# Kernel tuning notes

Hardware: AMD Instinct MI355X
Metric: run time of the kernel (lower is better)

## Reference

```python
import jax, jax.numpy as jnp
import numpy as np

THRESHOLD = 0.9
EPS = 1e-12  # F.normalize eps


def setup_inputs() -> dict:
    key = jax.random.key(0)
    clusters = jax.random.normal(key, (64, 256, 768), dtype=jnp.float32)
    return {"clusters": clusters}


def _collapse(clusters, threshold):
    B, Q, D = clusters.shape
    # F.normalize(clusters, dim=-1): divide by L2 norm clamped to eps
    norm = jnp.maximum(jnp.linalg.norm(clusters, axis=-1, keepdims=True), EPS)
    nc = clusters / norm
    sim = jnp.einsum('bqd,bkd->bqk', nc, nc)              # [B, Q, Q]
    # torch loop condition: collapse_mask[:, i, j].any() -> any over batch
    pair_flag = jnp.any(sim > threshold, axis=0)          # [Q, Q] bool, fixed before merging

    # loop order: i outer, j inner (j > i) == row-major upper triangle
    ii, jj = jnp.triu_indices(Q, k=1)
    flags = pair_flag[ii, jj]                              # [Q*(Q-1)/2]

    def step(c, x):
        i, j, f = x
        ci = jnp.take(c, i, axis=1)                        # [B, D]
        cj = jnp.take(c, j, axis=1)
        new_i = jnp.where(f, (ci + cj) * 0.5, ci)
        c = c.at[:, i].set(new_i)
        c = c.at[:, j].set(jnp.where(f, new_i, cj))        # clusters[:, j] = clusters[:, i]
        return c, None

    out, _ = jax.lax.scan(step, clusters, (ii, jj, flags))
    return out


def reference(clusters):
    return _collapse(clusters, THRESHOLD)
```

## Files before the change

kernel.cpp:

```cpp
#include <hip/hip_runtime.h>
#include <math.h>

#define BB 64
#define QQ 256
#define DD 768
#define THR 0.9f
#define EPSN 1e-12f

#define OFF_FBITS  0
#define OFF_COUNT  8192
#define OFF_PAIRS  8320
#define OFF_M      138880

using f32x4 = __attribute__((ext_vector_type(4))) float;
using s16x8 = __attribute__((ext_vector_type(8))) short;

struct Frag { float4 lo, hi; };

#define GL2LDS(g, l) __builtin_amdgcn_global_load_lds( \
    (const __attribute__((address_space(1))) void*)(g), \
    (__attribute__((address_space(3))) void*)(l), 16, 0, 0)

#define SCHED_FENCE() __builtin_amdgcn_sched_barrier(0)

__device__ __forceinline__ s16x8 cvt(const Frag& f) {
    union { s16x8 s; unsigned u[4]; } r;
    r.u[0] = __builtin_amdgcn_perm(__float_as_uint(f.lo.y), __float_as_uint(f.lo.x), 0x07060302u);
    r.u[1] = __builtin_amdgcn_perm(__float_as_uint(f.lo.w), __float_as_uint(f.lo.z), 0x07060302u);
    r.u[2] = __builtin_amdgcn_perm(__float_as_uint(f.hi.y), __float_as_uint(f.hi.x), 0x07060302u);
    r.u[3] = __builtin_amdgcn_perm(__float_as_uint(f.hi.w), __float_as_uint(f.hi.z), 0x07060302u);
    return r.s;
}
__device__ __forceinline__ float sq8(const Frag& f) {
    return f.lo.x*f.lo.x + f.lo.y*f.lo.y + f.lo.z*f.lo.z + f.lo.w*f.lo.w
         + f.hi.x*f.hi.x + f.hi.y*f.hi.y + f.hi.z*f.hi.z + f.hi.w*f.hi.w;
}

__global__ __launch_bounds__(256) void zero_kernel(unsigned* __restrict__ fbits,
                                                   int* __restrict__ count,
                                                   int* __restrict__ nflag) {
    int t = threadIdx.x;
    #pragma unroll
    for (int k = 0; k < 8; ++k) fbits[t + k * 256] = 0u;
    if (t == 0) { *count = 0; *nflag = 0; }
}

__global__ __launch_bounds__(256) void flags_kernel(const float* __restrict__ in,
                                                    float* __restrict__ out,
                                                    unsigned* __restrict__ fbits,
                                                    int* __restrict__ nflag) {
    __shared__ float lds[12288];

    int orig = blockIdx.x;
    int g = (orig & 7) * 80 + (orig >> 3);
    int tp = g % 10, b = g / 10;
    int it = 0, rem = tp, rowlen = 4;
    while (rem >= rowlen) { rem -= rowlen; ++it; --rowlen; }
    int jt = it + rem;
    int i0 = it * 64, j0 = jt * 64;

    int w = threadIdx.x >> 6, lane = threadIdx.x & 63;
    int wr = w >> 1, wc = w & 1;
    int r  = lane & 15, kg = lane >> 4;

    const float* base = in + (size_t)b * QQ * DD;

    int lr = lane >> 3;
    int lq = lane & 7;
    int swz = (lq ^ lr) * 4;
    const float* pA0 = base + (size_t)(i0 + w * 16 + lr) * DD + swz;
    const float* pA1 = pA0 + (size_t)8 * DD;
    const float* pB0 = base + (size_t)(j0 + w * 16 + lr) * DD + swz;
    const float* pB1 = pB0 + (size_t)8 * DD;

    f32x4 acc[2][2] = {};
    float4 ns = {0.f, 0.f, 0.f, 0.f};

    const f32x4* in4 = (const f32x4*)in;
    f32x4* out4 = (f32x4*)out;
    f32x4 cr[3];
    auto CLD = [&](int s) {
        int off = tp * 24 + s; off = off < 192 ? off : 191;
        cr[s % 3] = in4[(size_t)b * 49152 + (size_t)off * 256 + threadIdx.x];
    };
    auto CST = [&](int s) {
        int off = tp * 24 + s; off = off < 192 ? off : 191;
        out4[(size_t)b * 49152 + (size_t)off * 256 + threadIdx.x] = cr[s % 3];
    };

    auto STAGE = [&](int buf, int c) {
        int k0 = c * 32;
        float* L = lds + buf * 4096 + w * 512;
        GL2LDS(pA0 + k0, L);
        GL2LDS(pA1 + k0, L + 256);
        GL2LDS(pB0 + k0, L + 2048);
        GL2LDS(pB1 + k0, L + 2048 + 256);
    };
    auto RD = [&](const float* L, int row) {
        int qlo = (2 * kg) ^ (row & 7);
        Frag f;
        f.lo = *(const float4*)&L[row * 32 + qlo * 4];
        f.hi = *(const float4*)&L[row * 32 + (qlo ^ 1) * 4];
        return f;
    };
    auto CHUNK = [&](int buf) {
        const float* LA = lds + buf * 4096;
        const float* LB = LA + 2048;
        Frag fa0 = RD(LA, wr * 32 + r);
        Frag fa1 = RD(LA, wr * 32 + r + 16);
        Frag fb0 = RD(LB, wc * 32 + r);
        Frag fb1 = RD(LB, wc * 32 + r + 16);
        ns.x += sq8(fa0); ns.y += sq8(fa1); ns.z += sq8(fb0); ns.w += sq8(fb1);
        s16x8 a0 = cvt(fa0), a1 = cvt(fa1), b0 = cvt(fb0), b1 = cvt(fb1);
        acc[0][0] = __builtin_amdgcn_mfma_f32_16x16x32_bf16(a0, b0, acc[0][0], 0, 0, 0);
        acc[0][1] = __builtin_amdgcn_mfma_f32_16x16x32_bf16(a0, b1, acc[0][1], 0, 0, 0);
        acc[1][0] = __builtin_amdgcn_mfma_f32_16x16x32_bf16(a1, b0, acc[1][0], 0, 0, 0);
        acc[1][1] = __builtin_amdgcn_mfma_f32_16x16x32_bf16(a1, b1, acc[1][1], 0, 0, 0);
    };

    CLD(0); STAGE(0, 0);
    SCHED_FENCE();
    CLD(1); STAGE(1, 1);
    #pragma unroll
    for (int c = 0; c < 24; ++c) {
        SCHED_FENCE();
        if (c < 22) { CLD(c + 2); STAGE((c + 2) % 3, c + 2); }
        SCHED_FENCE();
        if (c == 0)       asm volatile("s_waitcnt vmcnt(10)");
        else if (c == 1)  asm volatile("s_waitcnt vmcnt(11)");
        else if (c <= 21) asm volatile("s_waitcnt vmcnt(12)");
        else if (c == 22) asm volatile("s_waitcnt vmcnt(7)");
        else              asm volatile("s_waitcnt vmcnt(2)");
        SCHED_FENCE();
        __builtin_amdgcn_s_barrier();
        CST(c);
        CHUNK(c % 3);
        SCHED_FENCE();
        __builtin_amdgcn_s_barrier();
    }

    ns.x += __shfl_xor(ns.x, 16); ns.x += __shfl_xor(ns.x, 32);
    ns.y += __shfl_xor(ns.y, 16); ns.y += __shfl_xor(ns.y, 32);
    ns.z += __shfl_xor(ns.z, 16); ns.z += __shfl_xor(ns.z, 32);
    ns.w += __shfl_xor(ns.w, 16); ns.w += __shfl_xor(ns.w, 32);

    float njc0 = fmaxf(sqrtf(ns.z), EPSN);
    float njc1 = fmaxf(sqrtf(ns.w), EPSN);

    bool any = false;
    #pragma unroll
    for (int m = 0; m < 2; ++m) {
        float nsa = (m == 0) ? ns.x : ns.y;
        #pragma unroll
        for (int rr = 0; rr < 4; ++rr) {
            float ni2 = __shfl(nsa, kg * 4 + rr);
            float ni  = fmaxf(sqrtf(ni2), EPSN);
            int i = i0 + wr * 32 + m * 16 + kg * 4 + rr;
            int j = j0 + wc * 32 + r;
            if (j > i && acc[m][0][rr] > THR * ni * njc0) {
                int idx = i * QQ + j;
                atomicOr(&fbits[idx >> 5], 1u << (idx & 31)); any = true;
            }
            j += 16;
            if (j > i && acc[m][1][rr] > THR * ni * njc1) {
                int idx = i * QQ + j;
                atomicOr(&fbits[idx >> 5], 1u << (idx & 31)); any = true;
            }
        }
    }
    if (any) atomicAdd(nflag, 1);
}

__global__ __launch_bounds__(256) void compact_merge_kernel(const unsigned* __restrict__ fbits,
                                                            int* __restrict__ pairs,
                                                            int* __restrict__ count,
                                                            const int* __restrict__ nflag,
                                                            float* __restrict__ M) {
    int t = threadIdx.x;
    if (*nflag == 0) { if (t == 0) *count = 0; return; }

    const int P  = QQ * (QQ - 1) / 2;
    const int CH = (P + 255) / 256;
    int L0 = t * CH;
    int L1 = min(L0 + CH, P);

    int i = 0, cum = 0;
    while (i < QQ - 1 && cum + (QQ - 1 - i) <= L0) { cum += (QQ - 1 - i); ++i; }
    int j = i + 1 + (L0 - cum);

    auto getbit = [&](int ii, int jj) -> int {
        int idx = ii * QQ + jj;
        return (fbits[idx >> 5] >> (idx & 31)) & 1;
    };

    int cnt = 0;
    { int ii = i, jj = j;
      for (int L = L0; L < L1; ++L) {
          cnt += getbit(ii, jj);
          if (++jj == QQ) { ++ii; jj = ii + 1; }
      } }

    __shared__ int sc[256];
    sc[t] = cnt;
    __syncthreads();
    for (int off = 1; off < 256; off <<= 1) {
        int u = (t >= off) ? sc[t - off] : 0;
        __syncthreads();
        sc[t] += u;
        __syncthreads();
    }
    int bse = sc[t] - cnt;
    if (t == 255) *count = sc[255];

    { int ii = i, jj = j;
      for (int L = L0; L < L1; ++L) {
          if (getbit(ii, jj)) pairs[bse++] = (ii << 16) | jj;
          if (++jj == QQ) { ++ii; jj = ii + 1; }
      } }
    __syncthreads();

    int n = sc[255];
    for (int rr = 0; rr < QQ; ++rr) M[rr * QQ + t] = (rr == t) ? 1.f : 0.f;
    for (int s = 0; s < n; ++s) {
        int pr = pairs[s];
        int pi = pr >> 16, pj = pr & 0xffff;
        float nv = 0.5f * (M[pi * QQ + t] + M[pj * QQ + t]);
        M[pi * QQ + t] = nv;
        M[pj * QQ + t] = nv;
    }
}

__global__ __launch_bounds__(256) void applyM_kernel(const float* __restrict__ in,
                                                     const float* __restrict__ M,
                                                     float* __restrict__ out,
                                                     const int* __restrict__ count) {
    if (*count == 0) return;
    int b = blockIdx.x, qt = blockIdx.y;
    int t = threadIdx.x;
    for (int q = qt * 64; q < qt * 64 + 64; ++q) {
        float a0 = 0.f, a1 = 0.f, a2 = 0.f;
        for (int k = 0; k < QQ; ++k) {
            float m = M[q * QQ + k];
            if (m == 0.f) continue;
            const float* src = in + ((size_t)b * QQ + k) * DD;
            a0 += m * src[t];
            a1 += m * src[t + 256];
            a2 += m * src[t + 512];
        }
        float* dst = out + ((size_t)b * QQ + q) * DD;
        dst[t] = a0; dst[t + 256] = a1; dst[t + 512] = a2;
    }
}

extern "C" void kernel_launch(void* const* d_in, const int* in_sizes, int n_in,
                              void* d_out, int out_size, void* d_ws, size_t ws_size,
                              hipStream_t stream) {
    const float* in = (const float*)d_in[0];
    float* out = (float*)d_out;
    char* ws = (char*)d_ws;

    unsigned* fbits = (unsigned*)(ws + OFF_FBITS);
    int*   count = (int*)  (ws + OFF_COUNT);
    int*   nflag = (int*)  (ws + OFF_COUNT + 4);
    int*   pairs = (int*)  (ws + OFF_PAIRS);
    float* M     = (float*)(ws + OFF_M);

    zero_kernel<<<dim3(1), dim3(256), 0, stream>>>(fbits, count, nflag);
    flags_kernel<<<dim3(640), dim3(256), 0, stream>>>(in, out, fbits, nflag);
    compact_merge_kernel<<<dim3(1), dim3(256), 0, stream>>>(fbits, pairs, count, nflag, M);
    applyM_kernel<<<dim3(BB, 4), dim3(256), 0, stream>>>(in, M, out, count);
}
```

Baseline: 39.51 us.

## Split Gram computation along D into halves and add separate threshold extraction kernel

Splits each per-batch 64x64 Gram tile computation across two blocks, each covering half of the D dimension, which doubles the grid to 1280 blocks and halves the per-block pipeline depth (double buffer instead of triple). Partial Gram tiles go to a workspace buffer, and row norms are accumulated with atomics from diagonal tiles. A new extract kernel sums the halves, normalizes and sets the pair flag bits. This aims for better occupancy and parallelism, at the cost of an extra kernel launch plus writing and reading the Gram tiles in global memory.

```diff
diff --git a/kernel.cpp b/kernel.cpp
--- a/kernel.cpp
+++ b/kernel.cpp
@@ -11,6 +11,9 @@
 #define OFF_COUNT  8192
 #define OFF_PAIRS  8320
 #define OFF_M      138880
+#define OFF_NSQ    401024
+#define OFF_G      466944
+#define GHALF      2621440
 
 using f32x4 = __attribute__((ext_vector_type(4))) float;
 using s16x8 = __attribute__((ext_vector_type(8))) short;
@@ -22,6 +25,16 @@
     (__attribute__((address_space(3))) void*)(l), 16, 0, 0)
 
 #define SCHED_FENCE() __builtin_amdgcn_sched_barrier(0)
+
+__device__ __forceinline__ void waitv(int n) {
+    if      (n >= 6)  asm volatile("s_waitcnt vmcnt(6)");
+    else if (n == 5)  asm volatile("s_waitcnt vmcnt(5)");
+    else if (n == 4)  asm volatile("s_waitcnt vmcnt(4)");
+    else if (n == 3)  asm volatile("s_waitcnt vmcnt(3)");
+    else if (n == 2)  asm volatile("s_waitcnt vmcnt(2)");
+    else if (n == 1)  asm volatile("s_waitcnt vmcnt(1)");
+    else              asm volatile("s_waitcnt vmcnt(0)");
+}
 
 __device__ __forceinline__ s16x8 cvt(const Frag& f) {
     union { s16x8 s; unsigned u[4]; } r;
@@ -38,35 +51,38 @@
 
 __global__ __launch_bounds__(256) void zero_kernel(unsigned* __restrict__ fbits,
                                                    int* __restrict__ count,
-                                                   int* __restrict__ nflag) {
-    int t = threadIdx.x;
+                                                   int* __restrict__ nflag,
+                                                   float* __restrict__ nsq) {
+    int t = threadIdx.x, blk = blockIdx.x;
+    fbits[blk * 256 + t] = 0u;
     #pragma unroll
-    for (int k = 0; k < 8; ++k) fbits[t + k * 256] = 0u;
-    if (t == 0) { *count = 0; *nflag = 0; }
-}
-
-__global__ __launch_bounds__(256) void flags_kernel(const float* __restrict__ in,
-                                                    float* __restrict__ out,
-                                                    unsigned* __restrict__ fbits,
-                                                    int* __restrict__ nflag) {
-    __shared__ float lds[12288];
+    for (int k = 0; k < 8; ++k) nsq[blk * 2048 + k * 256 + t] = 0.f;
+    if (blk == 0 && t == 0) { *count = 0; *nflag = 0; }
+}
+
+__global__ __launch_bounds__(256, 5) void gramh_kernel(const float* __restrict__ in,
+                                                       float* __restrict__ out,
+                                                       float* __restrict__ G,
+                                                       float* __restrict__ nsq) {
+    __shared__ float lds[8192];
 
     int orig = blockIdx.x;
-    int g = (orig & 7) * 80 + (orig >> 3);
-    int tp = g % 10, b = g / 10;
+    int g = (orig & 7) * 160 + (orig >> 3);
+    int p = g >> 1, h = g & 1;
+    int tp = p % 10, b = p / 10;
     int it = 0, rem = tp, rowlen = 4;
     while (rem >= rowlen) { rem -= rowlen; ++it; --rowlen; }
     int jt = it + rem;
     int i0 = it * 64, j0 = jt * 64;
 
-    int w = threadIdx.x >> 6, lane = threadIdx.x & 63;
+    int tid = threadIdx.x;
+    int w = tid >> 6, lane = tid & 63;
     int wr = w >> 1, wc = w & 1;
     int r  = lane & 15, kg = lane >> 4;
 
-    const float* base = in + (size_t)b * QQ * DD;
-
-    int lr = lane >> 3;
-    int lq = lane & 7;
+    const float* base = in + (size_t)b * QQ * DD + h * 384;
+
+    int lr = lane >> 3, lq = lane & 7;
     int swz = (lq ^ lr) * 4;
     const float* pA0 = base + (size_t)(i0 + w * 16 + lr) * DD + swz;
     const float* pA1 = pA0 + (size_t)8 * DD;
@@ -78,15 +94,14 @@
 
     const f32x4* in4 = (const f32x4*)in;
     f32x4* out4 = (f32x4*)out;
-    f32x4 cr[3];
-    auto CLD = [&](int s) {
-        int off = tp * 24 + s; off = off < 192 ? off : 191;
-        cr[s % 3] = in4[(size_t)b * 49152 + (size_t)off * 256 + threadIdx.x];
-    };
-    auto CST = [&](int s) {
-        int off = tp * 24 + s; off = off < 192 ? off : 191;
-        out4[(size_t)b * 49152 + (size_t)off * 256 + threadIdx.x] = cr[s % 3];
-    };
+    f32x4 cr[2];
+    int slotbase = tp * 20 + h * 10;
+    auto SLOT = [&](int s) -> size_t {
+        int idx = slotbase + s; idx = idx < 191 ? idx : 191;
+        return (size_t)b * 49152 + (size_t)idx * 256 + tid;
+    };
+    auto CLD = [&](int s) { cr[s & 1] = in4[SLOT(s)]; };
+    auto CST = [&](int s) { out4[SLOT(s)] = cr[s & 1]; };
 
     auto STAGE = [&](int buf, int c) {
         int k0 = c * 32;
@@ -119,52 +134,71 @@
     };
 
     CLD(0); STAGE(0, 0);
-    SCHED_FENCE();
-    CLD(1); STAGE(1, 1);
     #pragma unroll
-    for (int c = 0; c < 24; ++c) {
+    for (int c = 0; c < 12; ++c) {
         SCHED_FENCE();
-        if (c < 22) { CLD(c + 2); STAGE((c + 2) % 3, c + 2); }
+        if (c + 1 < 10) CLD(c + 1);
+        if (c + 1 < 12) STAGE((c + 1) & 1, c + 1);
         SCHED_FENCE();
-        if (c == 0)       asm volatile("s_waitcnt vmcnt(10)");
-        else if (c == 1)  asm volatile("s_waitcnt vmcnt(11)");
-        else if (c <= 21) asm volatile("s_waitcnt vmcnt(12)");
-        else if (c == 22) asm volatile("s_waitcnt vmcnt(7)");
-        else              asm volatile("s_waitcnt vmcnt(2)");
+        if (c == 0)       waitv(5);
+        else if (c <= 9)  waitv(6);
+        else if (c == 10) waitv(5);
+        else              waitv(0);
         SCHED_FENCE();
         __builtin_amdgcn_s_barrier();
-        CST(c);
-        CHUNK(c % 3);
+        CHUNK(c & 1);
+        if (c < 10) CST(c);
         SCHED_FENCE();
         __builtin_amdgcn_s_barrier();
     }
 
     ns.x += __shfl_xor(ns.x, 16); ns.x += __shfl_xor(ns.x, 32);
     ns.y += __shfl_xor(ns.y, 16); ns.y += __shfl_xor(ns.y, 32);
-    ns.z += __shfl_xor(ns.z, 16); ns.z += __shfl_xor(ns.z, 32);
-    ns.w += __shfl_xor(ns.w, 16); ns.w += __shfl_xor(ns.w, 32);
-
-    float njc0 = fmaxf(sqrtf(ns.z), EPSN);
-    float njc1 = fmaxf(sqrtf(ns.w), EPSN);
+    if (it == jt && wc == 0 && lane < 16) {
+        atomicAdd(&nsq[b * QQ + i0 + wr * 32 + lane], ns.x);
+        atomicAdd(&nsq[b * QQ + i0 + wr * 32 + 16 + lane], ns.y);
+    }
+
+    float* Gt = G + (h ? GHALF : 0) + (size_t)(tp * 64 + b) * 4096;
+    #pragma unroll
+    for (int m = 0; m < 2; ++m)
+        #pragma unroll
+        for (int n = 0; n < 2; ++n)
+            #pragma unroll
+            for (int rr = 0; rr < 4; ++rr)
+                Gt[(wr * 32 + m * 16 + kg * 4 + rr) * 64 + wc * 32 + n * 16 + r]
+                    = acc[m][n][rr];
+}
+
+__global__ __launch_bounds__(256) void extract_kernel(const float* __restrict__ G,
+                                                      const float* __restrict__ nsq,
+                                                      unsigned* __restrict__ fbits,
+                                                      int* __restrict__ nflag) {
+    int p = blockIdx.x;
+    int tp = p % 10, b = p / 10;
+    int it = 0, rem = tp, rowlen = 4;
+    while (rem >= rowlen) { rem -= rowlen; ++it; --rowlen; }
+    int jt = it + rem;
+    int i0 = it * 64, j0 = jt * 64;
+
+    const float* G0t = G + (size_t)(tp * 64 + b) * 4096;
+    const float* G1t = G0t + GHALF;
+    const float* nb = nsq + b * QQ;
 
     bool any = false;
     #pragma unroll
-    for (int m = 0; m < 2; ++m) {
-        float nsa = (m == 0) ? ns.x : ns.y;
-        #pragma unroll
-        for (int rr = 0; rr < 4; ++rr) {
-            float ni2 = __shfl(nsa, kg * 4 + rr);
-            float ni  = fmaxf(sqrtf(ni2), EPSN);
-            int i = i0 + wr * 32 + m * 16 + kg * 4 + rr;
-            int j = j0 + wc * 32 + r;
-            if (j > i && acc[m][0][rr] > THR * ni * njc0) {
+    for (int k = 0; k < 16; ++k) {
+        int e = k * 256 + threadIdx.x;
+        int il = e >> 6, jl = e & 63;
+        int i = i0 + il, j = j0 + jl;
+        if (j > i) {
+            float v = G0t[e] + G1t[e];
+            float ni = fmaxf(sqrtf(nb[i]), EPSN);
+            float nj = fmaxf(sqrtf(nb[j]), EPSN);
+            if (v > THR * ni * nj) {
                 int idx = i * QQ + j;
-                atomicOr(&fbits[idx >> 5], 1u << (idx & 31)); any = true;
-            }
-            j += 16;
-            if (j > i && acc[m][1][rr] > THR * ni * njc1) {
-                int idx = i * QQ + j;
-                atomicOr(&fbits[idx >> 5], 1u << (idx & 31)); any = true;
+                atomicOr(&fbits[idx >> 5], 1u << (idx & 31));
+                any = true;
             }
         }
     }
@@ -264,9 +298,12 @@
     int*   nflag = (int*)  (ws + OFF_COUNT + 4);
     int*   pairs = (int*)  (ws + OFF_PAIRS);
     float* M     = (float*)(ws + OFF_M);
-
-    zero_kernel<<<dim3(1), dim3(256), 0, stream>>>(fbits, count, nflag);
-    flags_kernel<<<dim3(640), dim3(256), 0, stream>>>(in, out, fbits, nflag);
+    float* nsq   = (float*)(ws + OFF_NSQ);
+    float* G     = (float*)(ws + OFF_G);
+
+    zero_kernel<<<dim3(8), dim3(256), 0, stream>>>(fbits, count, nflag, nsq);
+    gramh_kernel<<<dim3(1280), dim3(256), 0, stream>>>(in, out, G, nsq);
+    extract_kernel<<<dim3(640), dim3(256), 0, stream>>>(G, nsq, fbits, nflag);
     compact_merge_kernel<<<dim3(1), dim3(256), 0, stream>>>(fbits, pairs, count, nflag, M);
     applyM_kernel<<<dim3(BB, 4), dim3(256), 0, stream>>>(in, M, out, count);
 }
```

After: 47.38 us. +19.9%, slower.
